# Optimization experiments

Measured on AMD Instinct MI355X. Metric: run time of the kernel, lower is better.

## Reference

```python
import jax, jax.numpy as jnp
import numpy as np

D_MODEL = 1024
D_KV = 64
N_HEADS = 16
KV_HEADS = 4
G = N_HEADS // KV_HEADS
NUM_BUCKETS = 32
MAX_DISTANCE = 128


def _relative_position_bucket(relative_position, bidirectional=True,
                              num_buckets=NUM_BUCKETS, max_distance=MAX_DISTANCE):
    # Faithful port of T5Attention._relative_position_bucket
    relative_buckets = jnp.zeros_like(relative_position)
    if bidirectional:
        num_buckets //= 2
        relative_buckets = (relative_position > 0).astype(jnp.int32) * num_buckets
        relative_position = jnp.abs(relative_position)
    else:
        relative_position = -jnp.minimum(relative_position, 0)
    max_exact = num_buckets // 2
    is_small = relative_position < max_exact
    rel_if_large = max_exact + (
        jnp.log(relative_position.astype(jnp.float32) / max_exact)
        / np.log(max_distance / max_exact) * (num_buckets - max_exact)
    ).astype(jnp.int32)
    rel_if_large = jnp.minimum(rel_if_large, num_buckets - 1)
    return relative_buckets + jnp.where(is_small, relative_position, rel_if_large)


def setup_inputs() -> dict:
    key = jax.random.key(0)
    ks = jax.random.split(key, 6)
    B, S = 2, 2048
    inner = N_HEADS * D_KV
    sc = 1.0 / np.sqrt(D_MODEL)
    return {
        "hidden_states": jax.random.normal(ks[0], (B, S, D_MODEL), dtype=jnp.float32),
        "Wq": jax.random.normal(ks[1], (D_MODEL, inner), dtype=jnp.float32) * sc,
        "Wk": jax.random.normal(ks[2], (D_MODEL, inner), dtype=jnp.float32) * sc,
        "Wv": jax.random.normal(ks[3], (D_MODEL, inner), dtype=jnp.float32) * sc,
        "Wo": jax.random.normal(ks[4], (inner, D_MODEL), dtype=jnp.float32) * sc,
        "rel_bias": jax.random.normal(ks[5], (NUM_BUCKETS, N_HEADS), dtype=jnp.float32) * 0.1,
    }


def reference(hidden_states, Wq, Wk, Wv, Wo, rel_bias):
    B, S, _ = hidden_states.shape

    def split_heads(x):  # [B,S,inner] -> [B,H,S,Dk]
        return x.reshape(B, S, N_HEADS, D_KV).transpose(0, 2, 1, 3)

    q = split_heads(hidden_states @ Wq)
    k = split_heads(hidden_states @ Wk)
    v = split_heads(hidden_states @ Wv)

    # head index = g * KV_HEADS + h (einops 'b (g h) ...' with h=kv_heads)
    gq = q.reshape(B, G, KV_HEADS, S, D_KV)
    gk = k.reshape(B, G, KV_HEADS, S, D_KV).mean(axis=1)  # [B,Hkv,S,Dk]
    # einsum sums over g (as in torch.einsum 'bghnd,bhsd->bhns'); no 1/sqrt(d) in T5
    scores = jnp.einsum('bghnd,bhsd->bhns', gq, gk)  # [B,Hkv,S,S]

    # T5 relative position bias (bidirectional, encoder)
    ctx = jnp.arange(S)[:, None]
    mem = jnp.arange(S)[None, :]
    buckets = _relative_position_bucket(mem - ctx, bidirectional=True)
    bias = rel_bias[buckets]                # [S,S,H]
    bias = bias.transpose(2, 0, 1)[None]    # [1,H,S,S]
    gbias = bias.reshape(1, G, KV_HEADS, S, S).mean(axis=1)  # [1,Hkv,S,S]

    scores = scores + gbias
    attn = jax.nn.softmax(scores.astype(jnp.float32), axis=-1).astype(scores.dtype)

    # repeat grouped attn weights back to full heads: 'b h n s -> b (g h) n s'
    attn_full = jnp.tile(attn, (1, G, 1, 1))  # [B,H,S,S]
    ctx_out = jnp.einsum('bhns,bhsd->bhnd', attn_full, v)  # [B,H,S,Dk]
    ctx_out = ctx_out.transpose(0, 2, 1, 3).reshape(B, S, N_HEADS * D_KV)
    return ctx_out @ Wo  # [B,S,D_MODEL]
```

## Files before the change

kernel.cpp:

```cpp
#include <hip/hip_runtime.h>
#include <math.h>


typedef __bf16 bf16_t;
typedef bf16_t bf16x8 __attribute__((ext_vector_type(8)));
typedef bf16_t bf16x4 __attribute__((ext_vector_type(4)));
typedef float f32x4 __attribute__((ext_vector_type(4)));

#define MFMA16(a, b, c) __builtin_amdgcn_mfma_f32_16x16x32_bf16(a, b, c, 0, 0, 0)

typedef __attribute__((address_space(1))) void gvoid;
typedef __attribute__((address_space(3))) void svoid;
__device__ __forceinline__ void gld16(const void* g, void* l) {
    __builtin_amdgcn_global_load_lds((gvoid*)g, (svoid*)l, 16, 0, 0);
}

__global__ __launch_bounds__(256) void prep_all(const float* __restrict__ hs,
                                                const float* __restrict__ Wq,
                                                const float* __restrict__ Wk,
                                                const float* __restrict__ Wv,
                                                const float* __restrict__ Wo,
                                                const float* __restrict__ rel_bias,
                                                bf16_t* __restrict__ hs_hi,
                                                bf16_t* __restrict__ hs_lo,
                                                bf16_t* __restrict__ Thi,
                                                bf16_t* __restrict__ Tlo,
                                                bf16_t* __restrict__ WvT,
                                                bf16_t* __restrict__ WoT,
                                                float* __restrict__ btab) {
    __shared__ float sm[2048];
    const int r = blockIdx.x, t = threadIdx.x;
    if (r < 4096) {
        size_t idx = ((size_t)r * 256 + t) * 4;
        float4 v = *(const float4*)(hs + idx);
        bf16x4 h, l;
        h[0] = (bf16_t)v.x; l[0] = (bf16_t)(v.x - (float)h[0]);
        h[1] = (bf16_t)v.y; l[1] = (bf16_t)(v.y - (float)h[1]);
        h[2] = (bf16_t)v.z; l[2] = (bf16_t)(v.z - (float)h[2]);
        h[3] = (bf16_t)v.w; l[3] = (bf16_t)(v.w - (float)h[3]);
        *(bf16x4*)(hs_hi + idx) = h;
        *(bf16x4*)(hs_lo + idx) = l;
    } else if (r < 5120) {
        int k = r - 4096;
        float* rq = sm;
        float* rk = sm + 1024;
#pragma unroll
        for (int j = 0; j < 4; ++j) {
            rq[t + j * 256] = Wq[(size_t)k * 1024 + t + j * 256];
            rk[t + j * 256] = Wk[(size_t)k * 1024 + t + j * 256];
        }
        __syncthreads();
        int h = t >> 6, j2 = t & 63;
        float sq = 0.f, sk = 0.f;
#pragma unroll
        for (int g = 0; g < 4; ++g) {
            sq += rq[(g * 4 + h) * 64 + j2];
            sk += rk[(g * 4 + h) * 64 + j2];
        }
        sk *= 0.25f;
        bf16_t qh = (bf16_t)sq;
        Thi[(size_t)t * 1024 + k] = qh;
        Tlo[(size_t)t * 1024 + k] = (bf16_t)(sq - (float)qh);
        bf16_t kh = (bf16_t)sk;
        Thi[(size_t)(256 + t) * 1024 + k] = kh;
        Tlo[(size_t)(256 + t) * 1024 + k] = (bf16_t)(sk - (float)kh);
    } else if (r < 7168) {
        const float* src = (r < 6144) ? Wv : Wo;
        bf16_t* dst = (r < 6144) ? WvT : WoT;
        int rr = (r < 6144) ? r - 5120 : r - 6144;
        int bx = (rr & 31) * 32, by = (rr >> 5) * 32;
        int tx = t & 31, ty = t >> 5;
        float(*tile)[33] = (float(*)[33])sm;
#pragma unroll
        for (int i = 0; i < 32; i += 8)
            tile[ty + i][tx] = src[(size_t)(by + ty + i) * 1024 + bx + tx];
        __syncthreads();
#pragma unroll
        for (int i = 0; i < 32; i += 8)
            dst[(size_t)(bx + ty + i) * 1024 + by + tx] = (bf16_t)tile[tx][ty + i];
    } else {
        int idx = (r - 7168) * 256 + t;
        if (idx >= 4095) return;
        int delta = idx - 2047;
        int bucket = (delta > 0) ? 16 : 0;
        int arp = delta < 0 ? -delta : delta;
        int rb;
        if (arp < 8) {
            rb = arp;
        } else {
            float tt = (logf((float)arp * 0.125f) / 2.772588722239781f) * 8.0f;
            int ri = 8 + (int)tt;
            rb = ri < 15 ? ri : 15;
        }
        bucket += rb;
#pragma unroll
        for (int h = 0; h < 4; ++h) {
            float s = 0.25f * (rel_bias[bucket * 16 + h] + rel_bias[bucket * 16 + h + 4] +
                               rel_bias[bucket * 16 + h + 8] + rel_bias[bucket * 16 + h + 12]);
            btab[h * 4608 + idx] = s;
        }
    }
}

__global__ __launch_bounds__(256, 1) void proj_qkv(const bf16_t* __restrict__ Ah,
                                                   const bf16_t* __restrict__ Al,
                                                   const bf16_t* __restrict__ Bh,
                                                   const bf16_t* __restrict__ Bl,
                                                   const bf16_t* __restrict__ WvT,
                                                   bf16_t* __restrict__ Qhi,
                                                   bf16_t* __restrict__ Qlo,
                                                   bf16_t* __restrict__ Kbh,
                                                   bf16_t* __restrict__ Kbl,
                                                   bf16_t* __restrict__ Vb) {
    __shared__ bf16_t pool[24576];
    const int K = 1024, nk = 32;
    const int t = threadIdx.x;
    const int w = t >> 6, lane = t & 63;
    const int lr = lane & 15, q = lane >> 4;
    const int bx = blockIdx.x;
    const bool qk = bx < 8;
    const int m0 = blockIdx.y * 128;
    const int n0 = qk ? bx * 64 : (bx - 8) * 128;
    const int mw = (w & 1) * 64;
    f32x4 acc[4][4] = {};

    const int rA = t & 127, cA0 = t >> 7, cA1 = 2 + (t >> 7);
    const size_t oA0 = (size_t)(m0 + rA) * K + cA0 * 8;
    const size_t oA1 = (size_t)(m0 + rA) * K + cA1 * 8;
    const int rBq = t & 63, cBq = t >> 6;
    const size_t oBq = (size_t)(n0 + rBq) * K + cBq * 8;
    const size_t oBv0 = (size_t)(n0 + rA) * K + cA0 * 8;
    const size_t oBv1 = (size_t)(n0 + rA) * K + cA1 * 8;

    auto stage = [&](int bf, int k0) {
        gld16(Ah + oA0 + k0, &pool[bf * 4096 + t * 8]);
        gld16(Ah + oA1 + k0, &pool[bf * 4096 + (256 + t) * 8]);
        if (qk) {
            gld16(Al + oA0 + k0, &pool[8192 + bf * 4096 + t * 8]);
            gld16(Al + oA1 + k0, &pool[8192 + bf * 4096 + (256 + t) * 8]);
            gld16(Bh + oBq + k0, &pool[16384 + bf * 2048 + t * 8]);
            gld16(Bl + oBq + k0, &pool[20480 + bf * 2048 + t * 8]);
        } else {
            gld16(WvT + oBv0 + k0, &pool[8192 + bf * 4096 + t * 8]);
            gld16(WvT + oBv1 + k0, &pool[8192 + bf * 4096 + (256 + t) * 8]);
        }
    };

    stage(0, 0);
    __syncthreads();
    for (int it = 0; it < nk; ++it) {
        const int cur = it & 1;
        if (it + 1 < nk) stage(cur ^ 1, (it + 1) * 32);
        if (qk) {
            const int nw = (w >> 1) * 32;
            bf16x8 ah[4], al[4], bh[2], bl[2];
#pragma unroll
            for (int i = 0; i < 4; ++i) {
                int sa = (q * 128 + mw + i * 16 + lr) * 8;
                ah[i] = *(const bf16x8*)&pool[cur * 4096 + sa];
                al[i] = *(const bf16x8*)&pool[8192 + cur * 4096 + sa];
            }
#pragma unroll
            for (int j = 0; j < 2; ++j) {
                int sb = (q * 64 + nw + j * 16 + lr) * 8;
                bh[j] = *(const bf16x8*)&pool[16384 + cur * 2048 + sb];
                bl[j] = *(const bf16x8*)&pool[20480 + cur * 2048 + sb];
            }
#pragma unroll
            for (int i = 0; i < 4; ++i)
#pragma unroll
                for (int j = 0; j < 2; ++j) {
                    acc[i][j] = MFMA16(ah[i], bh[j], acc[i][j]);
                    acc[i][j] = MFMA16(ah[i], bl[j], acc[i][j]);
                    acc[i][j] = MFMA16(al[i], bh[j], acc[i][j]);
                }
        } else {
            const int nw = (w >> 1) * 64;
            bf16x8 af[4], bfv[4];
#pragma unroll
            for (int i = 0; i < 4; ++i)
                af[i] = *(const bf16x8*)&pool[cur * 4096 + (q * 128 + mw + i * 16 + lr) * 8];
#pragma unroll
            for (int j = 0; j < 4; ++j)
                bfv[j] =
                    *(const bf16x8*)&pool[8192 + cur * 4096 + (q * 128 + nw + j * 16 + lr) * 8];
#pragma unroll
            for (int i = 0; i < 4; ++i)
#pragma unroll
                for (int j = 0; j < 4; ++j) acc[i][j] = MFMA16(af[i], bfv[j], acc[i][j]);
        }
        __syncthreads();
    }

    const int nj = qk ? 2 : 4;
    const int nwq = qk ? (w >> 1) * 32 : (w >> 1) * 64;
#pragma unroll
    for (int i = 0; i < 4; ++i) {
        int row = m0 + mw + i * 16 + q * 4;
#pragma unroll 4
        for (int j = 0; j < nj; ++j) {
            int col = n0 + nwq + j * 16 + lr;
#pragma unroll
            for (int reg = 0; reg < 4; ++reg) {
                float x = acc[i][j][reg];
                int token = row + reg;
                if (qk) {
                    bf16_t hi = (bf16_t)x;
                    bf16_t lo = (bf16_t)(x - (float)hi);
                    if (col < 256) {
                        size_t o = (size_t)token * 256 + col;
                        Qhi[o] = hi;
                        Qlo[o] = lo;
                    } else {
                        int hc = col - 256;
                        int h = hc >> 6, d = hc & 63;
                        int b = token >> 11, s = token & 2047;
                        int it2 = s >> 6, sl = s & 63;
                        size_t o = ((size_t)((b * 4 + h) * 32 + it2)) * 4096 +
                                   (size_t)((d >> 3) * 64 + sl) * 8 + (d & 7);
                        Kbh[o] = hi;
                        Kbl[o] = lo;
                    }
                } else {
                    int vg = col;
                    int h = (vg >> 6) & 3, g = vg >> 8, d = vg & 63;
                    int b = token >> 11, s = token & 2047;
                    int it2 = s >> 6, sc = (s >> 3) & 7, si = s & 7;
                    size_t o = ((size_t)((b * 4 + h) * 32 + it2)) * 16384 +
                               (size_t)(sc * 256 + g * 64 + d) * 8 + si;
                    Vb[o] = (bf16_t)x;
                }
            }
        }
    }
}

__global__ __launch_bounds__(256, 1) void gemm_out(const bf16_t* __restrict__ A,
                                                   const bf16_t* __restrict__ BT,
                                                   float* __restrict__ C,
                                                   int M, int N, int K) {
    __shared__ bf16_t pool[12288];
    const int t = threadIdx.x;
    const int w = t >> 6, lane = t & 63;
    const int lr = lane & 15, q = lane >> 4;
    const int m0 = blockIdx.y * 128, n0 = blockIdx.x * 64;
    const int mw = (w & 1) * 64, nw = (w >> 1) * 32;
    f32x4 acc[4][2] = {};
    const int nk = K >> 5;

    const int rA = t & 127, cA0 = t >> 7, cA1 = 2 + (t >> 7);
    const bf16_t* gA0 = A + (size_t)(m0 + rA) * K + cA0 * 8;
    const bf16_t* gA1 = A + (size_t)(m0 + rA) * K + cA1 * 8;
    const bf16_t* gB = BT + (size_t)(n0 + (t & 63)) * K + (t >> 6) * 8;

    auto stage = [&](int bf, int k0) {
        gld16(gA0 + k0, &pool[bf * 4096 + t * 8]);
        gld16(gA1 + k0, &pool[bf * 4096 + (256 + t) * 8]);
        gld16(gB + k0, &pool[8192 + bf * 2048 + t * 8]);
    };

    stage(0, 0);
    __syncthreads();
    for (int it = 0; it < nk; ++it) {
        const int cur = it & 1;
        if (it + 1 < nk) stage(cur ^ 1, (it + 1) * 32);
        bf16x8 af[4], bfv[2];
#pragma unroll
        for (int i = 0; i < 4; ++i)
            af[i] = *(const bf16x8*)&pool[cur * 4096 + (q * 128 + mw + i * 16 + lr) * 8];
#pragma unroll
        for (int j = 0; j < 2; ++j)
            bfv[j] = *(const bf16x8*)&pool[8192 + cur * 2048 + (q * 64 + nw + j * 16 + lr) * 8];
#pragma unroll
        for (int i = 0; i < 4; ++i)
#pragma unroll
            for (int j = 0; j < 2; ++j) acc[i][j] = MFMA16(af[i], bfv[j], acc[i][j]);
        __syncthreads();
    }

#pragma unroll
    for (int i = 0; i < 4; ++i) {
        int row = m0 + mw + i * 16 + q * 4;
#pragma unroll
        for (int j = 0; j < 2; ++j) {
            int col = n0 + nw + j * 16 + lr;
#pragma unroll
            for (int reg = 0; reg < 4; ++reg)
                C[(size_t)(row + reg) * N + col] = acc[i][j][reg];
        }
    }
}

__global__ __launch_bounds__(512, 1) void attn_mfma(const bf16_t* __restrict__ Qhi,
                                                    const bf16_t* __restrict__ Qlo,
                                                    const bf16_t* __restrict__ Kbh,
                                                    const bf16_t* __restrict__ Kbl,
                                                    const bf16_t* __restrict__ Vb,
                                                    const float* __restrict__ btab,
                                                    bf16_t* __restrict__ part0,
                                                    bf16_t* __restrict__ part1,
                                                    float* __restrict__ Sml) {
    __shared__ bf16_t Kh[2][4096], Kl[2][4096], Vsm[2][16384], Ps[8192];
    const int t = threadIdx.x, w = t >> 6, lane = t & 63;
    const int lr = lane & 15, q = lane >> 4;
    const int blk = blockIdx.x;
    const int half = blk & 1, qt = (blk >> 1) & 15, h = (blk >> 5) & 3, b = blk >> 7;
    const int n0 = qt * 128;
    const int rowbase = n0 + w * 16;

    const size_t qrow = (size_t)(b * 2048 + rowbase + lr) * 256 + h * 64;
    bf16x8 aqh[2], aql[2];
#pragma unroll
    for (int kb = 0; kb < 2; ++kb) {
        aqh[kb] = *(const bf16x8*)(Qhi + qrow + kb * 32 + q * 8);
        aql[kb] = *(const bf16x8*)(Qlo + qrow + kb * 32 + q * 8);
    }

    const int tilebase = (b * 4 + h) * 32 + half * 16;
    const bf16_t* gK = Kbh + (size_t)tilebase * 4096;
    const bf16_t* gL = Kbl + (size_t)tilebase * 4096;
    const bf16_t* gV = Vb + (size_t)tilebase * 16384;
    const float* btabh = btab + h * 4608 + 2047;

    auto stage = [&](int bf, int it) {
        gld16(gK + (size_t)it * 4096 + t * 8, &Kh[bf][t * 8]);
        gld16(gL + (size_t)it * 4096 + t * 8, &Kl[bf][t * 8]);
        const bf16_t* v0 = gV + (size_t)it * 16384;
#pragma unroll
        for (int j = 0; j < 4; ++j)
            gld16(v0 + (j * 512 + t) * 8, &Vsm[bf][(j * 512 + t) * 8]);
    };

    float m_r[4], l_r[4];
#pragma unroll
    for (int reg = 0; reg < 4; ++reg) { m_r[reg] = -INFINITY; l_r[reg] = 0.f; }
    f32x4 O[16] = {};

    stage(0, 0);
    __syncthreads();
    for (int it = 0; it < 16; ++it) {
        const int cur = it & 1;
        if (it + 1 < 16) stage(cur ^ 1, it + 1);
        const int s0g = half * 1024 + it * 64;

        f32x4 sc[4];
#pragma unroll
        for (int ct = 0; ct < 4; ++ct) {
            f32x4 z = {0.f, 0.f, 0.f, 0.f};
#pragma unroll
            for (int kb = 0; kb < 2; ++kb) {
                int sb = ((kb * 4 + q) * 64 + ct * 16 + lr) * 8;
                bf16x8 bh = *(const bf16x8*)&Kh[cur][sb];
                bf16x8 bl = *(const bf16x8*)&Kl[cur][sb];
                z = MFMA16(aqh[kb], bh, z);
                z = MFMA16(aqh[kb], bl, z);
                z = MFMA16(aql[kb], bh, z);
            }
            sc[ct] = z;
        }
        const int dbase = (s0g + lr) - (rowbase + q * 4);
#pragma unroll
        for (int ct = 0; ct < 4; ++ct)
#pragma unroll
            for (int reg = 0; reg < 4; ++reg)
                sc[ct][reg] += btabh[dbase + ct * 16 - reg];

        float rm[4];
#pragma unroll
        for (int reg = 0; reg < 4; ++reg)
            rm[reg] = fmaxf(fmaxf(sc[0][reg], sc[1][reg]), fmaxf(sc[2][reg], sc[3][reg]));
#pragma unroll
        for (int off = 1; off < 16; off <<= 1)
#pragma unroll
            for (int reg = 0; reg < 4; ++reg)
                rm[reg] = fmaxf(rm[reg], __shfl_xor(rm[reg], off, 64));

        float alpha[4], rs[4];
#pragma unroll
        for (int reg = 0; reg < 4; ++reg) {
            float mo = m_r[reg];
            float mn = fmaxf(mo, rm[reg]);
            alpha[reg] = __expf(mo - mn);
            m_r[reg] = mn;
            rs[reg] = 0.f;
        }
#pragma unroll
        for (int ct = 0; ct < 4; ++ct) {
#pragma unroll
            for (int reg = 0; reg < 4; ++reg) {
                float p = __expf(sc[ct][reg] - m_r[reg]);
                rs[reg] += p;
                int col = ct * 16 + lr;
                Ps[((w * 128 + (col >> 3) * 16) + q * 4 + reg) * 8 + (col & 7)] = (bf16_t)p;
            }
        }
#pragma unroll
        for (int off = 1; off < 16; off <<= 1)
#pragma unroll
            for (int reg = 0; reg < 4; ++reg) rs[reg] += __shfl_xor(rs[reg], off, 64);
#pragma unroll
        for (int reg = 0; reg < 4; ++reg) l_r[reg] = l_r[reg] * alpha[reg] + rs[reg];

        bf16x8 pa[2];
#pragma unroll
        for (int kb = 0; kb < 2; ++kb)
            pa[kb] = *(const bf16x8*)&Ps[(w * 128 + (kb * 4 + q) * 16 + lr) * 8];

#pragma unroll
        for (int nt = 0; nt < 16; ++nt) {
            f32x4 o = O[nt];
#pragma unroll
            for (int reg = 0; reg < 4; ++reg) o[reg] *= alpha[reg];
#pragma unroll
            for (int kb = 0; kb < 2; ++kb) {
                bf16x8 v = *(const bf16x8*)&Vsm[cur][((kb * 4 + q) * 256 + nt * 16 + lr) * 8];
                o = MFMA16(pa[kb], v, o);
            }
            O[nt] = o;
        }
        __syncthreads();
    }

    bf16_t* P = half ? part1 : part0;
    float inv[4];
#pragma unroll
    for (int reg = 0; reg < 4; ++reg) inv[reg] = 1.f / l_r[reg];
    const size_t tokbase = (size_t)(b * 2048 + rowbase + q * 4);
#pragma unroll
    for (int nt = 0; nt < 16; ++nt) {
        int v = nt * 16 + lr;
        int vg = ((v >> 6) * 4 + h) * 64 + (v & 63);
#pragma unroll
        for (int reg = 0; reg < 4; ++reg)
            P[(tokbase + reg) * 1024 + vg] = (bf16_t)(O[nt][reg] * inv[reg]);
    }
    if (lr == 0) {
#pragma unroll
        for (int reg = 0; reg < 4; ++reg)
            Sml[half * 16384 + (tokbase + reg) * 4 + h] = m_r[reg] + logf(l_r[reg]);
    }
}

__global__ __launch_bounds__(256) void combine_halves(bf16_t* __restrict__ p0,
                                                      const bf16_t* __restrict__ p1,
                                                      const float* __restrict__ Sml) {
    size_t flat = ((size_t)blockIdx.x * 256 + threadIdx.x) * 8;
    int tok = (int)(flat >> 10), c = (int)(flat & 1023), h = (c >> 6) & 3;
    float s0 = Sml[tok * 4 + h], s1 = Sml[16384 + tok * 4 + h];
    float M = fmaxf(s0, s1);
    float e0 = __expf(s0 - M), e1 = __expf(s1 - M);
    float r = 1.f / (e0 + e1);
    float w0 = e0 * r, w1 = e1 * r;
    bf16x8 a = *(bf16x8*)(p0 + flat);
    bf16x8 bb = *(const bf16x8*)(p1 + flat);
    bf16x8 o;
#pragma unroll
    for (int i = 0; i < 8; ++i) o[i] = (bf16_t)(w0 * (float)a[i] + w1 * (float)bb[i]);
    *(bf16x8*)(p0 + flat) = o;
}

extern "C" void kernel_launch(void* const* d_in, const int* in_sizes, int n_in,
                              void* d_out, int out_size, void* d_ws, size_t ws_size,
                              hipStream_t stream) {
    const float* hs = (const float*)d_in[0];
    const float* Wq = (const float*)d_in[1];
    const float* Wk = (const float*)d_in[2];
    const float* Wv = (const float*)d_in[3];
    const float* Wo = (const float*)d_in[4];
    const float* rb = (const float*)d_in[5];
    float* out = (float*)d_out;

    const size_t MB = 1 << 20;
    const size_t KB = 1 << 10;
    char* ws = (char*)d_ws;
    bf16_t* hs_hi = (bf16_t*)(ws);
    bf16_t* hs_lo = (bf16_t*)(ws + 8 * MB);
    bf16_t* WqkThi = (bf16_t*)(ws + 16 * MB);
    bf16_t* WqkTlo = (bf16_t*)(ws + 17 * MB);
    bf16_t* WvT = (bf16_t*)(ws + 18 * MB);
    bf16_t* WoT = (bf16_t*)(ws + 20 * MB);
    float* btab = (float*)(ws + 22 * MB);
    float* Sml = (float*)(ws + 22 * MB + 128 * KB);
    bf16_t* Qhi = (bf16_t*)(ws + 22 * MB + 256 * KB);
    bf16_t* Qlo = Qhi + (size_t)4096 * 256;
    bf16_t* Kbh = Qlo + (size_t)4096 * 256;
    bf16_t* Kbl = Kbh + (size_t)4096 * 256;
    bf16_t* Vb = Kbl + (size_t)4096 * 256;
    bf16_t* part0 = hs_hi;
    bf16_t* part1 = hs_lo;

    prep_all<<<7184, 256, 0, stream>>>(hs, Wq, Wk, Wv, Wo, rb, hs_hi, hs_lo, WqkThi,
                                       WqkTlo, WvT, WoT, btab);
    proj_qkv<<<dim3(16, 32), 256, 0, stream>>>(hs_hi, hs_lo, WqkThi, WqkTlo, WvT, Qhi,
                                               Qlo, Kbh, Kbl, Vb);
    attn_mfma<<<256, 512, 0, stream>>>(Qhi, Qlo, Kbh, Kbl, Vb, btab, part0, part1, Sml);
    combine_halves<<<2048, 256, 0, stream>>>(part0, part1, Sml);
    gemm_out<<<dim3(16, 32), 256, 0, stream>>>(part0, WoT, out, 4096, 1024, 1024);
}
```

Before: 239.6 us.

## Transpose attention MFMA operands so each lane owns one query row

Swaps the A/B operands of the QK and PV MFMAs so the score tile is transposed and each lane holds a single query row. This replaces the per-register 4-stage shuffle reductions for row max and sum with two cross-quad shuffles and scalar softmax state. P is written to LDS as packed bf16x4 stores with an XOR swizzle instead of scalar scattered stores. The output goes through a swizzled LDS staging pass so global writes are 16-byte coalesced rows. The per-lane bias indexing and output layout become more intricate, which adds risk of indexing errors.

```diff
diff --git a/kernel.cpp b/kernel.cpp
--- a/kernel.cpp
+++ b/kernel.cpp
@@ -307,6 +307,8 @@
     const int half = blk & 1, qt = (blk >> 1) & 15, h = (blk >> 5) & 3, b = blk >> 7;
     const int n0 = qt * 128;
     const int rowbase = n0 + w * 16;
+    const int swz = (lr & 7) << 3;
+    const int psb = w * 1024 + lr * 64;
 
     const size_t qrow = (size_t)(b * 2048 + rowbase + lr) * 256 + h * 64;
     bf16x8 aqh[2], aql[2];
@@ -331,9 +333,7 @@
             gld16(v0 + (j * 512 + t) * 8, &Vsm[bf][(j * 512 + t) * 8]);
     };
 
-    float m_r[4], l_r[4];
-#pragma unroll
-    for (int reg = 0; reg < 4; ++reg) { m_r[reg] = -INFINITY; l_r[reg] = 0.f; }
+    float m_r = -INFINITY, l_r = 0.f;
     f32x4 O[16] = {};
 
     stage(0, 0);
@@ -352,93 +352,84 @@
                 int sb = ((kb * 4 + q) * 64 + ct * 16 + lr) * 8;
                 bf16x8 bh = *(const bf16x8*)&Kh[cur][sb];
                 bf16x8 bl = *(const bf16x8*)&Kl[cur][sb];
-                z = MFMA16(aqh[kb], bh, z);
-                z = MFMA16(aqh[kb], bl, z);
-                z = MFMA16(aql[kb], bh, z);
+                z = MFMA16(bh, aqh[kb], z);
+                z = MFMA16(bh, aql[kb], z);
+                z = MFMA16(bl, aqh[kb], z);
             }
             sc[ct] = z;
         }
-        const int dbase = (s0g + lr) - (rowbase + q * 4);
+        const int dbase = (s0g + q * 4) - (rowbase + lr);
 #pragma unroll
         for (int ct = 0; ct < 4; ++ct)
 #pragma unroll
             for (int reg = 0; reg < 4; ++reg)
-                sc[ct][reg] += btabh[dbase + ct * 16 - reg];
-
-        float rm[4];
-#pragma unroll
-        for (int reg = 0; reg < 4; ++reg)
-            rm[reg] = fmaxf(fmaxf(sc[0][reg], sc[1][reg]), fmaxf(sc[2][reg], sc[3][reg]));
-#pragma unroll
-        for (int off = 1; off < 16; off <<= 1)
-#pragma unroll
-            for (int reg = 0; reg < 4; ++reg)
-                rm[reg] = fmaxf(rm[reg], __shfl_xor(rm[reg], off, 64));
-
-        float alpha[4], rs[4];
-#pragma unroll
-        for (int reg = 0; reg < 4; ++reg) {
-            float mo = m_r[reg];
-            float mn = fmaxf(mo, rm[reg]);
-            alpha[reg] = __expf(mo - mn);
-            m_r[reg] = mn;
-            rs[reg] = 0.f;
-        }
+                sc[ct][reg] += btabh[dbase + ct * 16 + reg];
+
+        float mt = fmaxf(fmaxf(sc[0][0], sc[0][1]), fmaxf(sc[0][2], sc[0][3]));
+#pragma unroll
+        for (int ct = 1; ct < 4; ++ct)
+            mt = fmaxf(mt, fmaxf(fmaxf(sc[ct][0], sc[ct][1]), fmaxf(sc[ct][2], sc[ct][3])));
+        mt = fmaxf(mt, __shfl_xor(mt, 16, 64));
+        mt = fmaxf(mt, __shfl_xor(mt, 32, 64));
+
+        float mn = fmaxf(m_r, mt);
+        float al = __expf(m_r - mn);
+        m_r = mn;
+        float rs = 0.f;
 #pragma unroll
         for (int ct = 0; ct < 4; ++ct) {
+            bf16x4 tq;
 #pragma unroll
             for (int reg = 0; reg < 4; ++reg) {
-                float p = __expf(sc[ct][reg] - m_r[reg]);
-                rs[reg] += p;
-                int col = ct * 16 + lr;
-                Ps[((w * 128 + (col >> 3) * 16) + q * 4 + reg) * 8 + (col & 7)] = (bf16_t)p;
+                float p = __expf(sc[ct][reg] - mn);
+                rs += p;
+                tq[reg] = (bf16_t)p;
             }
-        }
-#pragma unroll
-        for (int off = 1; off < 16; off <<= 1)
-#pragma unroll
-            for (int reg = 0; reg < 4; ++reg) rs[reg] += __shfl_xor(rs[reg], off, 64);
-#pragma unroll
-        for (int reg = 0; reg < 4; ++reg) l_r[reg] = l_r[reg] * alpha[reg] + rs[reg];
-
-        bf16x8 pa[2];
-#pragma unroll
-        for (int kb = 0; kb < 2; ++kb)
-            pa[kb] = *(const bf16x8*)&Ps[(w * 128 + (kb * 4 + q) * 16 + lr) * 8];
+            *(bf16x4*)&Ps[psb + ((ct * 16 + q * 4) ^ swz)] = tq;
+        }
+        rs += __shfl_xor(rs, 16, 64);
+        rs += __shfl_xor(rs, 32, 64);
+        l_r = l_r * al + rs;
+
+        bf16x8 pf0 = *(const bf16x8*)&Ps[psb + ((q * 8) ^ swz)];
+        bf16x8 pf1 = *(const bf16x8*)&Ps[psb + ((32 + q * 8) ^ swz)];
 
 #pragma unroll
         for (int nt = 0; nt < 16; ++nt) {
             f32x4 o = O[nt];
 #pragma unroll
-            for (int reg = 0; reg < 4; ++reg) o[reg] *= alpha[reg];
-#pragma unroll
-            for (int kb = 0; kb < 2; ++kb) {
-                bf16x8 v = *(const bf16x8*)&Vsm[cur][((kb * 4 + q) * 256 + nt * 16 + lr) * 8];
-                o = MFMA16(pa[kb], v, o);
-            }
+            for (int reg = 0; reg < 4; ++reg) o[reg] *= al;
+            bf16x8 v0 = *(const bf16x8*)&Vsm[cur][(q * 256 + nt * 16 + lr) * 8];
+            o = MFMA16(v0, pf0, o);
+            bf16x8 v1 = *(const bf16x8*)&Vsm[cur][((4 + q) * 256 + nt * 16 + lr) * 8];
+            o = MFMA16(v1, pf1, o);
             O[nt] = o;
         }
         __syncthreads();
     }
 
     bf16_t* P = half ? part1 : part0;
-    float inv[4];
-#pragma unroll
-    for (int reg = 0; reg < 4; ++reg) inv[reg] = 1.f / l_r[reg];
-    const size_t tokbase = (size_t)(b * 2048 + rowbase + q * 4);
-#pragma unroll
-    for (int nt = 0; nt < 16; ++nt) {
-        int v = nt * 16 + lr;
-        int vg = ((v >> 6) * 4 + h) * 64 + (v & 63);
-#pragma unroll
-        for (int reg = 0; reg < 4; ++reg)
-            P[(tokbase + reg) * 1024 + vg] = (bf16_t)(O[nt][reg] * inv[reg]);
-    }
-    if (lr == 0) {
-#pragma unroll
-        for (int reg = 0; reg < 4; ++reg)
-            Sml[half * 16384 + (tokbase + reg) * 4 + h] = m_r[reg] + logf(l_r[reg]);
-    }
+    const float inv = 1.f / l_r;
+    const int tokb = b * 2048 + rowbase;
+#pragma unroll
+    for (int G = 0; G < 4; ++G) {
+#pragma unroll
+        for (int g4 = 0; g4 < 4; ++g4) {
+            int nt = G * 4 + g4;
+            bf16x4 tq;
+#pragma unroll
+            for (int reg = 0; reg < 4; ++reg) tq[reg] = (bf16_t)(O[nt][reg] * inv);
+            *(bf16x4*)&Ps[psb + ((g4 * 16 + q * 4) ^ swz)] = tq;
+        }
+#pragma unroll
+        for (int i = 0; i < 2; ++i) {
+            int row = i * 8 + (lane >> 3), cv = (lane & 7) * 8;
+            bf16x8 fr = *(const bf16x8*)&Ps[w * 1024 + row * 64 + (cv ^ ((row & 7) << 3))];
+            *(bf16x8*)(P + (size_t)(tokb + row) * 1024 + (G * 4 + h) * 64 + cv) = fr;
+        }
+    }
+    if (lane < 16)
+        Sml[half * 16384 + (size_t)(tokb + lane) * 4 + h] = m_r + logf(l_r);
 }
 
 __global__ __launch_bounds__(256) void combine_halves(bf16_t* __restrict__ p0,
```

Measured after the change: 229.5 us. 4.2% less time.
